# Kernel optimization log

Measured on AMD Instinct MI355X. Metric: run time of the kernel, lower is better.

The kernel has to match this reference:

```python
import jax, jax.numpy as jnp
import numpy as np

IN_DIM = 128
DIM = 32

def setup_inputs() -> dict:
    key = jax.random.key(0)
    ks = jax.random.split(key, 7)
    b, r, L = 1, 128, 256
    m = jax.random.normal(ks[0], (b, r, L, IN_DIM), dtype=jnp.float32)
    ln_w = jnp.ones((IN_DIM,), dtype=jnp.float32)
    ln_b = jnp.zeros((IN_DIM,), dtype=jnp.float32)
    W1 = jax.random.normal(ks[1], (2 * DIM, IN_DIM), dtype=jnp.float32) / np.sqrt(IN_DIM)
    b1 = jax.random.normal(ks[2], (2 * DIM,), dtype=jnp.float32) * 0.01
    W2 = jax.random.normal(ks[3], (IN_DIM, DIM * DIM), dtype=jnp.float32) / np.sqrt(DIM * DIM)
    b2 = jax.random.normal(ks[4], (IN_DIM,), dtype=jnp.float32) * 0.01
    return {"m": m, "ln_w": ln_w, "ln_b": ln_b, "W1": W1, "b1": b1, "W2": W2, "b2": b2}

def reference(m, ln_w, ln_b, W1, b1, W2, b2):
    nrow = m.shape[1]
    # LayerNorm over last dim
    mu = jnp.mean(m, axis=-1, keepdims=True)
    var = jnp.var(m, axis=-1, keepdims=True)
    mn = (m - mu) / jnp.sqrt(var + 1e-5) * ln_w + ln_b
    # projection to a, b (chunk on last dim)
    proj = jnp.einsum('bric,fc->brif', mn, W1) + b1  # [b,r,L,2*DIM]
    a, bb = proj[..., :DIM], proj[..., DIM:]
    # outer-product mean over rows r
    out = jnp.einsum('bric,brjd->bijcd', a, bb) / nrow  # [b,L,L,DIM,DIM]
    B, I, J = out.shape[0], out.shape[1], out.shape[2]
    out = out.reshape(B, I, J, DIM * DIM)
    z = jnp.einsum('bijk,fk->bijf', out, W2) + b2  # [b,L,L,IN_DIM]
    return z
```

## Files before the change

### kernel.cpp

```cpp
#include <hip/hip_runtime.h>
#include <stdint.h>

typedef __attribute__((ext_vector_type(8)))  short short8;
typedef __attribute__((ext_vector_type(4)))  float f32x4;
typedef __attribute__((ext_vector_type(16))) float f32x16;

static __device__ __forceinline__ uint32_t f2bf(float x) {
    union { float f; uint32_t u; } v; v.f = x;
    return (v.u + 0x7FFFu + ((v.u >> 16) & 1u)) >> 16;
}


__global__ __launch_bounds__(256) void prep_weights(
    const float* __restrict__ W2, const float* __restrict__ W1,
    uint16_t* __restrict__ W2f, uint16_t* __restrict__ W1f) {
    int bid = blockIdx.x, t = threadIdx.x;
    if (bid < 512) {
        int idx = bid * 256 + t;
        int f  = idx >> 10;
        int kd = idx & 1023;
        int d = kd >> 5, c = kd & 31;
        int ft = f >> 5, r32 = f & 31;
        int ks16 = kd >> 4, kh32 = (kd >> 3) & 1, e = kd & 7;
        W2f[(size_t)(ft * 64 + ks16) * 512 + (r32 + 32 * kh32) * 8 + e] =
            (uint16_t)f2bf(W2[f * 1024 + c * 32 + d]);
    } else {
        int idx = (bid - 512) * 256 + t;
        int f = idx >> 7, c = idx & 127;
        int ftile = f >> 4, l16 = f & 15;
        int ks = c >> 5, kh = (c >> 3) & 3, e = c & 7;
        W1f[(size_t)(ftile * 4 + ks) * 512 + (l16 + 16 * kh) * 8 + e] =
            (uint16_t)f2bf(W1[f * 128 + c]);
    }
}

__global__ __launch_bounds__(256) void ln_proj(
    const float* __restrict__ mI, const float* __restrict__ lnw,
    const float* __restrict__ lnb, const uint16_t* __restrict__ W1f,
    const float* __restrict__ b1,
    uint16_t* __restrict__ At, uint16_t* __restrict__ Bt)
{
    __shared__ __align__(16) uint16_t mns[256 * 8];
    const int t = threadIdx.x;
    const int bid = blockIdx.x;
    const int i0 = (bid * 16) & 255;
    const int r  = bid >> 4;

    {
        int row = t >> 4, cb = t & 15;
        const float* rp = mI + ((size_t)bid * 16 + row) * 128 + cb * 8;
        float4 v0 = *(const float4*)(rp);
        float4 v1 = *(const float4*)(rp + 4);
        float s  = v0.x + v0.y + v0.z + v0.w + v1.x + v1.y + v1.z + v1.w;
        float ss = v0.x*v0.x + v0.y*v0.y + v0.z*v0.z + v0.w*v0.w
                 + v1.x*v1.x + v1.y*v1.y + v1.z*v1.z + v1.w*v1.w;
        #pragma unroll
        for (int off = 8; off > 0; off >>= 1) {
            s  += __shfl_xor(s, off);
            ss += __shfl_xor(ss, off);
        }
        float mean = s * (1.0f / 128.0f);
        float var  = ss * (1.0f / 128.0f) - mean * mean;
        float rstd = rsqrtf(var + 1e-5f);
        float4 wa = *(const float4*)(lnw + cb * 8);
        float4 wb = *(const float4*)(lnw + cb * 8 + 4);
        float4 ba = *(const float4*)(lnb + cb * 8);
        float4 bb = *(const float4*)(lnb + cb * 8 + 4);
        uint16_t y[8];
        y[0] = (uint16_t)f2bf((v0.x - mean) * rstd * wa.x + ba.x);
        y[1] = (uint16_t)f2bf((v0.y - mean) * rstd * wa.y + ba.y);
        y[2] = (uint16_t)f2bf((v0.z - mean) * rstd * wa.z + ba.z);
        y[3] = (uint16_t)f2bf((v0.w - mean) * rstd * wa.w + ba.w);
        y[4] = (uint16_t)f2bf((v1.x - mean) * rstd * wb.x + bb.x);
        y[5] = (uint16_t)f2bf((v1.y - mean) * rstd * wb.y + bb.y);
        y[6] = (uint16_t)f2bf((v1.z - mean) * rstd * wb.z + bb.z);
        y[7] = (uint16_t)f2bf((v1.w - mean) * rstd * wb.w + bb.w);
        int g = cb * 16 + (row ^ (cb & 7));
        *(uint2*)&mns[g * 8]     = *(uint2*)&y[0];
        *(uint2*)&mns[g * 8 + 4] = *(uint2*)&y[4];
    }
    __syncthreads();

    const int w = t >> 6, l = t & 63;
    const int l16 = l & 15, lh = l >> 4;
    f32x4 acc = (f32x4)(0.0f);
    #pragma unroll
    for (int ks = 0; ks < 4; ++ks) {
        int cb = ks * 4 + lh;
        int g  = cb * 16 + (l16 ^ (cb & 7));
        short8 a = *(const short8*)&mns[g * 8];
        short8 b = *(const short8*)(W1f + (size_t)(w * 4 + ks) * 512 + l * 8);
        acc = __builtin_amdgcn_mfma_f32_16x16x32_bf16(a, b, acc, 0, 0, 0);
    }
    float b1v = b1[w * 16 + l16];
    uint16_t* dst = (w < 2) ? At : Bt;
    const float scale = (w < 2) ? (1.0f / 128.0f) : 1.0f;
    const int cch = w & 1;
    const int base2 = (r >> 5) * 512 + (l16 + 16 * ((r >> 3) & 3)) * 8 + (r & 7);
    #pragma unroll
    for (int v = 0; v < 4; ++v) {
        int i = i0 + lh * 4 + v;
        int mtile = i * 2 + cch;
        dst[(size_t)mtile * 2048 + base2] = (uint16_t)f2bf((acc[v] + b1v) * scale);
    }
}

extern __shared__ uint16_t outl[];
__global__ __launch_bounds__(512, 4) void fused_opm(
    const uint16_t* __restrict__ At, const uint16_t* __restrict__ Bt,
    const uint16_t* __restrict__ W2f, const float* __restrict__ b2,
    float* __restrict__ z)
{
    const int t = threadIdx.x;
    const int w = t >> 6, l = t & 63;
    const int l16 = l & 15, lh = l >> 4;
    const int bx = blockIdx.x, by = blockIdx.y;
    const int wm = w >> 1, wn = w & 1;

    f32x4 acc[4][4];
    #pragma unroll
    for (int a = 0; a < 4; ++a)
        #pragma unroll
        for (int b = 0; b < 4; ++b) acc[a][b] = (f32x4)(0.0f);

    const uint16_t* Abase = At + (size_t)(by * 16 + wm * 4) * 4 * 512 + l * 8;
    const uint16_t* Bbase = Bt + (size_t)(bx * 8 + wn * 4) * 4 * 512 + l * 8;
    #pragma unroll
    for (int ks = 0; ks < 4; ++ks) {
        short8 af[4], bf[4];
        #pragma unroll
        for (int mt = 0; mt < 4; ++mt)
            af[mt] = *(const short8*)(Abase + (size_t)(mt * 4 + ks) * 512);
        #pragma unroll
        for (int nt = 0; nt < 4; ++nt)
            bf[nt] = *(const short8*)(Bbase + (size_t)(nt * 4 + ks) * 512);
        #pragma unroll
        for (int mt = 0; mt < 4; ++mt)
            #pragma unroll
            for (int nt = 0; nt < 4; ++nt)
                acc[mt][nt] = __builtin_amdgcn_mfma_f32_16x16x32_bf16(
                    af[mt], bf[nt], acc[mt][nt], 0, 0, 0);
    }

    const int h32 = w >> 2;
    const int ft  = w & 3;
    const uint16_t* Wt = W2f + ((size_t)ft * 64 + (size_t)h32 * 32) * 512 + l * 8;
    short8 wbuf[4];
    #pragma unroll
    for (int q = 0; q < 4; ++q)
        wbuf[q] = *(const short8*)(Wt + (size_t)q * 512);

    {
        const int kh32w = lh >> 1;
        const uint32_t e0b = (uint32_t)((lh & 1) * 4) * 2u;
        #pragma unroll
        for (int mt = 0; mt < 4; ++mt) {
            #pragma unroll
            for (int nt = 0; nt < 4; ++nt) {
                int p    = wm * 8 + (mt >> 1) * 4 + wn * 2 + (nt >> 1);
                int d    = (nt & 1) * 16 + l16;
                int ks16 = 2 * d + (mt & 1);
                f32x4 v = acc[mt][nt];
                uint2 pk;
                pk.x = f2bf(v[0]) | (f2bf(v[1]) << 16);
                pk.y = f2bf(v[2]) | (f2bf(v[3]) << 16);
                uint32_t off = (uint32_t)(p + 32 * kh32w) * 16u + e0b;
                off ^= ((uint32_t)((ks16 & 7) ^ kh32w)) << 4;
                *(uint2*)((char*)outl + (uint32_t)ks16 * 1024u + off) = pk;
            }
        }
    }
    __syncthreads();

    f32x16 zacc0 = (f32x16)(0.0f), zacc1 = (f32x16)(0.0f);
    const int kh32r = l >> 5;
    #pragma unroll
    for (int it = 0; it < 32; ++it) {
        short8 cw = wbuf[it & 3];
        if (it < 28) wbuf[it & 3] = *(const short8*)(Wt + (size_t)(it + 4) * 512);
        int ks16 = h32 * 32 + it;
        uint32_t off = ((uint32_t)l * 16u) ^ (((uint32_t)((ks16 & 7) ^ kh32r)) << 4);
        short8 o = *(const short8*)((const char*)outl + (uint32_t)ks16 * 1024u + off);
        if (it & 1) zacc1 = __builtin_amdgcn_mfma_f32_32x32x16_bf16(cw, o, zacc1, 0, 0, 0);
        else        zacc0 = __builtin_amdgcn_mfma_f32_32x32x16_bf16(cw, o, zacc0, 0, 0, 0);
    }

    float part[16];
    #pragma unroll
    for (int rr = 0; rr < 16; ++rr) part[rr] = zacc0[rr] + zacc1[rr];

    __syncthreads();
    float* red = (float*)outl;
    if (w >= 4) {
        #pragma unroll
        for (int rr = 0; rr < 16; ++rr)
            red[(ft * 16 + rr) * 64 + l] = part[rr];
    }
    __syncthreads();
    if (w < 4) {
        #pragma unroll
        for (int rr = 0; rr < 16; ++rr)
            part[rr] += red[(ft * 16 + rr) * 64 + l];
        const int p  = l & 31;
        const int zi = by * 8 + (p >> 2);
        const int zj = bx * 4 + (p & 3);
        float* zrow = z + ((size_t)zi * 256 + zj) * 128;
        #pragma unroll
        for (int rq = 0; rq < 4; ++rq) {
            int f0 = ft * 32 + rq * 8 + 4 * (l >> 5);
            float4 bv = *(const float4*)(b2 + f0);
            float4 zr;
            zr.x = part[rq * 4 + 0] + bv.x;
            zr.y = part[rq * 4 + 1] + bv.y;
            zr.z = part[rq * 4 + 2] + bv.z;
            zr.w = part[rq * 4 + 3] + bv.w;
            *(float4*)(zrow + f0) = zr;
        }
    }
}

extern "C" void kernel_launch(void* const* d_in, const int* in_sizes, int n_in,
                              void* d_out, int out_size, void* d_ws, size_t ws_size,
                              hipStream_t stream) {
    const float* m_in = (const float*)d_in[0];
    const float* ln_w = (const float*)d_in[1];
    const float* ln_b = (const float*)d_in[2];
    const float* W1   = (const float*)d_in[3];
    const float* b1   = (const float*)d_in[4];
    const float* W2   = (const float*)d_in[5];
    const float* b2   = (const float*)d_in[6];
    float* z = (float*)d_out;

    uint16_t* At  = (uint16_t*)d_ws;
    uint16_t* Bt  = At + 8192 * 128;
    uint16_t* W2f = Bt + 8192 * 128;
    uint16_t* W1f = W2f + 128 * 1024;

    prep_weights<<<544, 256, 0, stream>>>(W2, W1, W2f, W1f);
    ln_proj<<<2048, 256, 0, stream>>>(m_in, ln_w, ln_b, W1f, b1, At, Bt);
    fused_opm<<<dim3(64, 32), 512, 64 * 1024, stream>>>(At, Bt, W2f, b2, z);
}
```

Baseline: 69.75 us.

## Split second GEMM over output features with 16x16 MFMA, drop cross-wave reduction

The W2 projection stage is re-partitioned. Each of the 8 waves now owns a 16-position tile and two 16-feature output tiles over the full K=1024, using 16x16x32 MFMAs, instead of 32x32x16 MFMAs split over K halves. This removes the LDS partial-sum reduction, its two extra barriers and the idle half of the waves in the epilogue. In exchange each wave loads twice as many W2 fragments from global memory per K step, the W2 prep layout and LDS layout change to match, and the smaller MFMA shape has lower per-instruction throughput.

```diff
diff --git a/kernel.cpp b/kernel.cpp
--- a/kernel.cpp
+++ b/kernel.cpp
@@ -1,9 +1,8 @@
 #include <hip/hip_runtime.h>
 #include <stdint.h>
 
-typedef __attribute__((ext_vector_type(8)))  short short8;
-typedef __attribute__((ext_vector_type(4)))  float f32x4;
-typedef __attribute__((ext_vector_type(16))) float f32x16;
+typedef __attribute__((ext_vector_type(8))) short  short8;
+typedef __attribute__((ext_vector_type(4))) float  f32x4;
 
 static __device__ __forceinline__ uint32_t f2bf(float x) {
     union { float f; uint32_t u; } v; v.f = x;
@@ -20,9 +19,9 @@
         int f  = idx >> 10;
         int kd = idx & 1023;
         int d = kd >> 5, c = kd & 31;
-        int ft = f >> 5, r32 = f & 31;
-        int ks16 = kd >> 4, kh32 = (kd >> 3) & 1, e = kd & 7;
-        W2f[(size_t)(ft * 64 + ks16) * 512 + (r32 + 32 * kh32) * 8 + e] =
+        int ftile = f >> 4, l16 = f & 15;
+        int ks = kd >> 5, kh = (kd >> 3) & 3, e = kd & 7;
+        W2f[(size_t)(ftile * 32 + ks) * 512 + (l16 + 16 * kh) * 8 + e] =
             (uint16_t)f2bf(W2[f * 1024 + c * 32 + d]);
     } else {
         int idx = (bid - 512) * 256 + t;
@@ -142,80 +141,80 @@
                     af[mt], bf[nt], acc[mt][nt], 0, 0, 0);
     }
 
-    const int h32 = w >> 2;
-    const int ft  = w & 3;
-    const uint16_t* Wt = W2f + ((size_t)ft * 64 + (size_t)h32 * 32) * 512 + l * 8;
-    short8 wbuf[4];
-    #pragma unroll
-    for (int q = 0; q < 4; ++q)
-        wbuf[q] = *(const short8*)(Wt + (size_t)q * 512);
-
+    const int pt  = w & 1;
+    const int ft0 = (w >> 1) * 2;
+    const uint16_t* Wt0 = W2f + (size_t)(ft0    ) * 32 * 512 + l * 8;
+    const uint16_t* Wt1 = W2f + (size_t)(ft0 + 1) * 32 * 512 + l * 8;
+    short8 wb0[4], wb1[4];
+    #pragma unroll
+    for (int q = 0; q < 4; ++q) {
+        wb0[q] = *(const short8*)(Wt0 + (size_t)q * 512);
+        wb1[q] = *(const short8*)(Wt1 + (size_t)q * 512);
+    }
+
+    #pragma unroll
+    for (int mt = 0; mt < 4; ++mt) {
+        const int kh = (mt & 1) * 2 + (lh >> 1);
+        const int e0 = (lh & 1) * 4;
+        #pragma unroll
+        for (int nt = 0; nt < 4; ++nt) {
+            int p  = wm * 8 + (mt >> 1) * 4 + wn * 2 + (nt >> 1);
+            int ks = (nt & 1) * 16 + l16;
+            int ptw = p >> 4, l16t = p & 15;
+            f32x4 v = acc[mt][nt];
+            uint2 pk;
+            pk.x = f2bf(v[0]) | (f2bf(v[1]) << 16);
+            pk.y = f2bf(v[2]) | (f2bf(v[3]) << 16);
+            uint32_t byte = (uint32_t)(ptw * 32 + ks) * 1024u
+                          + (uint32_t)(l16t + 16 * kh) * 16u + (uint32_t)e0 * 2u;
+            byte ^= (uint32_t)(ks & 7) << 4;
+            *(uint2*)((char*)outl + byte) = pk;
+        }
+    }
+    __syncthreads();
+
+    f32x4 zacc0[2], zacc1[2];
+    zacc0[0] = (f32x4)(0.0f); zacc0[1] = (f32x4)(0.0f);
+    zacc1[0] = (f32x4)(0.0f); zacc1[1] = (f32x4)(0.0f);
+
+    #pragma unroll
+    for (int ks = 0; ks < 32; ++ks) {
+        short8 cw0 = wb0[ks & 3];
+        short8 cw1 = wb1[ks & 3];
+        if (ks < 28) {
+            wb0[ks & 3] = *(const short8*)(Wt0 + (size_t)(ks + 4) * 512);
+            wb1[ks & 3] = *(const short8*)(Wt1 + (size_t)(ks + 4) * 512);
+        }
+        uint32_t ob = ((uint32_t)(pt * 32 + ks) * 1024u + (uint32_t)l * 16u)
+                    ^ ((uint32_t)(ks & 7) << 4);
+        short8 o = *(const short8*)((const char*)outl + ob);
+        zacc0[ks & 1] = __builtin_amdgcn_mfma_f32_16x16x32_bf16(cw0, o, zacc0[ks & 1], 0, 0, 0);
+        zacc1[ks & 1] = __builtin_amdgcn_mfma_f32_16x16x32_bf16(cw1, o, zacc1[ks & 1], 0, 0, 0);
+    }
+
+    const int p  = pt * 16 + l16;
+    const int zi = by * 8 + (p >> 2);
+    const int zj = bx * 4 + (p & 3);
+    float* zrow = z + ((size_t)zi * 256 + zj) * 128;
     {
-        const int kh32w = lh >> 1;
-        const uint32_t e0b = (uint32_t)((lh & 1) * 4) * 2u;
-        #pragma unroll
-        for (int mt = 0; mt < 4; ++mt) {
-            #pragma unroll
-            for (int nt = 0; nt < 4; ++nt) {
-                int p    = wm * 8 + (mt >> 1) * 4 + wn * 2 + (nt >> 1);
-                int d    = (nt & 1) * 16 + l16;
-                int ks16 = 2 * d + (mt & 1);
-                f32x4 v = acc[mt][nt];
-                uint2 pk;
-                pk.x = f2bf(v[0]) | (f2bf(v[1]) << 16);
-                pk.y = f2bf(v[2]) | (f2bf(v[3]) << 16);
-                uint32_t off = (uint32_t)(p + 32 * kh32w) * 16u + e0b;
-                off ^= ((uint32_t)((ks16 & 7) ^ kh32w)) << 4;
-                *(uint2*)((char*)outl + (uint32_t)ks16 * 1024u + off) = pk;
-            }
-        }
-    }
-    __syncthreads();
-
-    f32x16 zacc0 = (f32x16)(0.0f), zacc1 = (f32x16)(0.0f);
-    const int kh32r = l >> 5;
-    #pragma unroll
-    for (int it = 0; it < 32; ++it) {
-        short8 cw = wbuf[it & 3];
-        if (it < 28) wbuf[it & 3] = *(const short8*)(Wt + (size_t)(it + 4) * 512);
-        int ks16 = h32 * 32 + it;
-        uint32_t off = ((uint32_t)l * 16u) ^ (((uint32_t)((ks16 & 7) ^ kh32r)) << 4);
-        short8 o = *(const short8*)((const char*)outl + (uint32_t)ks16 * 1024u + off);
-        if (it & 1) zacc1 = __builtin_amdgcn_mfma_f32_32x32x16_bf16(cw, o, zacc1, 0, 0, 0);
-        else        zacc0 = __builtin_amdgcn_mfma_f32_32x32x16_bf16(cw, o, zacc0, 0, 0, 0);
-    }
-
-    float part[16];
-    #pragma unroll
-    for (int rr = 0; rr < 16; ++rr) part[rr] = zacc0[rr] + zacc1[rr];
-
-    __syncthreads();
-    float* red = (float*)outl;
-    if (w >= 4) {
-        #pragma unroll
-        for (int rr = 0; rr < 16; ++rr)
-            red[(ft * 16 + rr) * 64 + l] = part[rr];
-    }
-    __syncthreads();
-    if (w < 4) {
-        #pragma unroll
-        for (int rr = 0; rr < 16; ++rr)
-            part[rr] += red[(ft * 16 + rr) * 64 + l];
-        const int p  = l & 31;
-        const int zi = by * 8 + (p >> 2);
-        const int zj = bx * 4 + (p & 3);
-        float* zrow = z + ((size_t)zi * 256 + zj) * 128;
-        #pragma unroll
-        for (int rq = 0; rq < 4; ++rq) {
-            int f0 = ft * 32 + rq * 8 + 4 * (l >> 5);
-            float4 bv = *(const float4*)(b2 + f0);
-            float4 zr;
-            zr.x = part[rq * 4 + 0] + bv.x;
-            zr.y = part[rq * 4 + 1] + bv.y;
-            zr.z = part[rq * 4 + 2] + bv.z;
-            zr.w = part[rq * 4 + 3] + bv.w;
-            *(float4*)(zrow + f0) = zr;
-        }
+        int f0 = ft0 * 16 + lh * 4;
+        float4 bv = *(const float4*)(b2 + f0);
+        float4 zr;
+        zr.x = zacc0[0][0] + zacc0[1][0] + bv.x;
+        zr.y = zacc0[0][1] + zacc0[1][1] + bv.y;
+        zr.z = zacc0[0][2] + zacc0[1][2] + bv.z;
+        zr.w = zacc0[0][3] + zacc0[1][3] + bv.w;
+        *(float4*)(zrow + f0) = zr;
+    }
+    {
+        int f0 = (ft0 + 1) * 16 + lh * 4;
+        float4 bv = *(const float4*)(b2 + f0);
+        float4 zr;
+        zr.x = zacc1[0][0] + zacc1[1][0] + bv.x;
+        zr.y = zacc1[0][1] + zacc1[1][1] + bv.y;
+        zr.z = zacc1[0][2] + zacc1[1][2] + bv.z;
+        zr.w = zacc1[0][3] + zacc1[1][3] + bv.w;
+        *(float4*)(zrow + f0) = zr;
     }
 }
 
```

New measurement: 75.53 us. 8.3% more time.
